# Optimization experiments

Measured on AMD Instinct MI355X. Metric: run time of the kernel, lower is better.

## Reference

```python
import jax, jax.numpy as jnp
from jax import lax
import numpy as np

HID = 1000


def _lstm_cell(x, h, c, W_ih, W_hh, b_ih, b_hh):
    # PyTorch nn.LSTMCell gate order: i, f, g, o
    gates = x @ W_ih.T + b_ih + h @ W_hh.T + b_hh  # [B, 4H]
    i, f, g, o = jnp.split(gates, 4, axis=-1)
    c2 = jax.nn.sigmoid(f) * c + jax.nn.sigmoid(i) * jnp.tanh(g)
    h2 = jax.nn.sigmoid(o) * jnp.tanh(c2)
    return h2, c2


def setup_inputs() -> dict:
    key = jax.random.key(0)
    ks = jax.random.split(key, 8)
    B, T, nbones = 256, 49, 64
    D = nbones * 3
    s = 0.05
    inp = {"enc_in": jax.random.normal(ks[0], (B, T, D), jnp.float32)}
    dims = [D, HID, HID]
    for l in range(3):
        inp[f"W_ih{l}"] = jax.random.normal(ks[1 + 2 * l], (4 * HID, dims[l]), jnp.float32) * s
        inp[f"W_hh{l}"] = jax.random.normal(ks[2 + 2 * l], (4 * HID, HID), jnp.float32) * s
        inp[f"b_ih{l}"] = jnp.zeros((4 * HID,), jnp.float32)
        inp[f"b_hh{l}"] = jnp.zeros((4 * HID,), jnp.float32)
    inp["train"] = 0  # eval mode: dropout is identity
    return inp


def reference(enc_in, W_ih0, W_hh0, b_ih0, b_hh0,
              W_ih1, W_hh1, b_ih1, b_hh1,
              W_ih2, W_hh2, b_ih2, b_hh2, train):
    params = [(W_ih0, W_hh0, b_ih0, b_hh0),
              (W_ih1, W_hh1, b_ih1, b_hh1),
              (W_ih2, W_hh2, b_ih2, b_hh2)]
    B = enc_in.shape[0]
    zeros = jnp.zeros((B, HID), enc_in.dtype)
    init = (tuple(zeros for _ in range(3)), tuple(zeros for _ in range(3)))

    def step(carry, x):
        hs, cs = carry
        new_h, new_c = [], []
        inp = x
        for l in range(3):
            h2, c2 = _lstm_cell(inp, hs[l], cs[l], *params[l])
            new_h.append(h2)
            new_c.append(c2)
            inp = h2  # dropout with train=False is identity
        return (tuple(new_h), tuple(new_c)), jnp.stack(new_h)  # [3, B, H]

    # scan over time: enc_in [B, T, D] -> [T, B, D]
    _, ys = lax.scan(step, init, jnp.transpose(enc_in, (1, 0, 2)))
    # ys: [T, 3, B, H] -> [3, B, T, H]; equals the original per-layer `output`
    out = jnp.transpose(ys, (1, 2, 0, 3))
    return out
```

## Files before the change

kernel.cpp:

```cpp
#include <hip/hip_runtime.h>

#define HID_ 1000
#define NB 256
#define TT 49
#define DIN 192
#define NPAD 1024
#define M_ALL (TT * 256)

typedef _Float16 f16;
typedef _Float16 f16x4 __attribute__((ext_vector_type(4)));
typedef _Float16 f16x8 __attribute__((ext_vector_type(8)));
typedef float f32x4 __attribute__((ext_vector_type(4)));
typedef const __attribute__((address_space(1))) unsigned int* gas_u32;
typedef __attribute__((address_space(3))) unsigned int* las_u32;

__device__ __forceinline__ float sigmf_(float x) {
    return 1.0f / (1.0f + __expf(-x));
}
__device__ __forceinline__ float tanhf_(float x) {
    float ax = fabsf(x);
    float e = __expf(-2.0f * ax);
    float t = (1.0f - e) / (1.0f + e);
    return copysignf(t, x);
}

__global__ void conv_weight(const float* __restrict__ src, f16* __restrict__ dst,
                            int K, int KPADv) {
    size_t total = 4ull * NPAD * KPADv;
    for (size_t idx = (size_t)blockIdx.x * blockDim.x + threadIdx.x; idx < total;
         idx += (size_t)gridDim.x * blockDim.x) {
        int kp = (int)(idx % KPADv);
        size_t rest = idx / KPADv;
        int np = (int)(rest % NPAD);
        int g = (int)(rest / NPAD);
        f16 v = (f16)0.0f;
        if (np < HID_ && kp < K) v = (f16)src[(size_t)(g * HID_ + np) * K + kp];
        dst[idx] = v;
    }
}

__global__ void conv_x(const float* __restrict__ src, f16* __restrict__ dst) {
    size_t total = (size_t)TT * NB * DIN;
    for (size_t idx = (size_t)blockIdx.x * blockDim.x + threadIdx.x; idx < total;
         idx += (size_t)gridDim.x * blockDim.x) {
        int k = (int)(idx % DIN);
        size_t rest = idx / DIN;
        int b = (int)(rest % NB);
        int t = (int)(rest / NB);
        dst[idx] = (f16)src[((size_t)b * TT + t) * DIN + k];
    }
}

__global__ void conv_bias(const float* __restrict__ bih, const float* __restrict__ bhh,
                          float* __restrict__ dst) {
    int idx = blockIdx.x * blockDim.x + threadIdx.x;
    if (idx < 4 * NPAD) {
        int np = idx & (NPAD - 1);
        int g = idx >> 10;
        float v = 0.0f;
        if (np < HID_) v = bih[g * HID_ + np] + bhh[g * HID_ + np];
        dst[idx] = v;
    }
}

__global__ __launch_bounds__(256) void input_gemm(
    const f16* __restrict__ A, int lda, int kiters,
    const f16* __restrict__ W, int ldw,
    const float* __restrict__ bias,
    f16* __restrict__ pre2) {
    __shared__ f16 As[128 * 64];
    __shared__ f16 Bs[128 * 64];
    const int id = blockIdx.x;
    const int sw = (id & 7) * (gridDim.x >> 3) + (id >> 3);
    const int m0 = (sw >> 5) << 7;
    const int n0 = (sw & 31) << 7;
    const int w = threadIdx.x >> 6;
    const int lane = threadIdx.x & 63;
    const int r = lane & 15;
    const int u = lane >> 4;
    const int kb8 = u << 3;
    const int wm = (w >> 1) << 6, wn = (w & 1) << 6;
    const int strow = (w << 5) + (lane >> 3);
    const int stcol = (lane & 7) << 3;

    f32x4 acc[4][4];
#pragma unroll
    for (int i = 0; i < 4; i++)
#pragma unroll
        for (int j = 0; j < 4; j++) acc[i][j] = (f32x4){0.f, 0.f, 0.f, 0.f};

    for (int kt = 0; kt < kiters; kt++) {
        const int k0 = kt << 6;
#pragma unroll
        for (int q = 0; q < 4; q++) {
            const int row = strow + (q << 3);
            const int cbase = ((w << 5) + (q << 3)) << 6;
            const f16* ga = A + (size_t)(m0 + row) * lda + k0 + stcol;
            const f16* gb = W + (size_t)(n0 + row) * ldw + k0 + stcol;
            __builtin_amdgcn_global_load_lds((gas_u32)ga, (las_u32)(As + cbase), 16, 0, 0);
            __builtin_amdgcn_global_load_lds((gas_u32)gb, (las_u32)(Bs + cbase), 16, 0, 0);
        }
        __syncthreads();
#pragma unroll
        for (int ks = 0; ks < 2; ks++) {
            f16x8 av[4], bv[4];
#pragma unroll
            for (int i = 0; i < 4; i++)
                av[i] = *(const f16x8*)(As + ((wm + i * 16 + r) << 6) + (ks << 5) + kb8);
#pragma unroll
            for (int j = 0; j < 4; j++)
                bv[j] = *(const f16x8*)(Bs + ((wn + j * 16 + r) << 6) + (ks << 5) + kb8);
#pragma unroll
            for (int i = 0; i < 4; i++)
#pragma unroll
                for (int j = 0; j < 4; j++)
                    acc[i][j] = __builtin_amdgcn_mfma_f32_16x16x32_f16(av[i], bv[j], acc[i][j], 0, 0, 0);
        }
        __syncthreads();
    }

#pragma unroll
    for (int j = 0; j < 4; j++) {
        const int gcol = n0 + wn + j * 16 + r;
        const float bj = bias[gcol];
        const int g = gcol >> 10;
        const int cl = gcol & 1023;
        const int jt2 = cl >> 5;
        const int n2 = (cl >> 4) & 1;
#pragma unroll
        for (int i = 0; i < 4; i++) {
            const int grow = m0 + wm + i * 16 + (u << 2);
            const int t_ = grow >> 8;
            const int bt2 = (grow >> 5) & 7;
            const int mi = i & 1;
            f16x4 hv;
#pragma unroll
            for (int q = 0; q < 4; q++) hv[q] = (f16)(acc[i][j][q] + bj);
            const int slot = (u << 4) + r;
            *(f16x4*)(pre2 + (((size_t)t_ * 8 + bt2) * 32 + jt2) * 4096 +
                      (size_t)slot * 64 + g * 16 + n2 * 8 + mi * 4) = hv;
        }
    }
}

__global__ __launch_bounds__(512, 2) void rec_persist(
    const f16* __restrict__ Whh, const f16* __restrict__ pre2,
    f16* __restrict__ hall, float* __restrict__ outl,
    unsigned int* __restrict__ flags) {
    __shared__ __align__(16) char smem[64 * 1024];
    __shared__ float pl[4 * 4 * 32 * 34];
    const int bid = blockIdx.x;
    const int bt = bid & 7;
    const int jt = bid >> 3;
    const int b0 = bt << 5;
    const int jc0 = jt << 5;
    const int tid = threadIdx.x;
    const int w = tid >> 6;
    const int gp = w >> 2;
    const int kh = w & 3;
    const int lane = tid & 63;
    const int r = lane & 15;
    const int u = lane >> 4;
    const int swz = (r & 7) << 4;

    f16x8 wreg[2][2][8];
#pragma unroll
    for (int gl = 0; gl < 2; gl++)
#pragma unroll
        for (int n = 0; n < 2; n++) {
            const f16* wp = Whh + ((size_t)((2 * gp + gl) * NPAD + jc0 + n * 16 + r)) * NPAD +
                            (kh << 8) + (u << 3);
#pragma unroll
            for (int ks = 0; ks < 8; ks++) wreg[gl][n][ks] = *(const f16x8*)(wp + ks * 32);
        }

    const int eb = tid >> 4;
    const int ej = (tid & 15) << 1;
    float cv[2] = {0.f, 0.f};
    unsigned int* myflags = flags + bt * TT;
    const size_t preblk = (((size_t)bt * 32 + jt) * 4096) + (size_t)lane * 64 + gp * 32;

    auto LOADP = [&](int tindex, f16x8 (&pc)[4]) {
        if (kh == 0) {
            const f16* pp = pre2 + (size_t)tindex * 8 * 32 * 4096 + preblk;
#pragma unroll
            for (int c = 0; c < 4; c++) pc[c] = *(const f16x8*)(pp + c * 8);
        }
    };

    auto STEP = [&](int t, f16x8 (&pc)[4], f16x8 (&pn)[4]) {
        LOADP(t + 1 < TT ? t + 1 : t, pn);

        if (t > 0) {
            while (__hip_atomic_load(myflags + (t - 1), __ATOMIC_RELAXED,
                                     __HIP_MEMORY_SCOPE_AGENT) < 32u) {}
            asm volatile("" ::: "memory");
            const char* hread = (const char*)(hall + (size_t)(t - 1) * NB * NPAD);
#pragma unroll
            for (int i = 0; i < 8; i++) {
                const int c = tid + (i << 9);
                const int row = c >> 7;
                const int cb = (c & 127) << 4;
                const char* gsrc = hread + ((size_t)(b0 + row) << 11) + (cb ^ ((row & 7) << 4));
                __builtin_amdgcn_global_load_lds((gas_u32)gsrc,
                                                 (las_u32)(smem + (w << 10) + (i << 13)), 16, 0, 0);
            }
        }
        __syncthreads();

        f32x4 acc[2][2][2];
#pragma unroll
        for (int mi = 0; mi < 2; mi++)
#pragma unroll
            for (int gl = 0; gl < 2; gl++)
#pragma unroll
                for (int n = 0; n < 2; n++)
#pragma unroll
                    for (int q = 0; q < 4; q++)
                        acc[mi][gl][n][q] = (kh == 0) ? (float)pc[gl * 2 + n][mi * 4 + q] : 0.f;

        if (t > 0) {
#pragma unroll
            for (int ks = 0; ks < 8; ks++) {
                const int kb = ((kh * 8 + ks) << 6) + (u << 4);
                f16x8 a0 = *(const f16x8*)(smem + r * 2048 + (kb ^ swz));
                f16x8 a1 = *(const f16x8*)(smem + (16 + r) * 2048 + (kb ^ swz));
#pragma unroll
                for (int gl = 0; gl < 2; gl++)
#pragma unroll
                    for (int n = 0; n < 2; n++) {
                        acc[0][gl][n] = __builtin_amdgcn_mfma_f32_16x16x32_f16(
                            a0, wreg[gl][n][ks], acc[0][gl][n], 0, 0, 0);
                        acc[1][gl][n] = __builtin_amdgcn_mfma_f32_16x16x32_f16(
                            a1, wreg[gl][n][ks], acc[1][gl][n], 0, 0, 0);
                    }
            }
        }
#pragma unroll
        for (int mi = 0; mi < 2; mi++)
#pragma unroll
            for (int gl = 0; gl < 2; gl++)
#pragma unroll
                for (int n = 0; n < 2; n++)
#pragma unroll
                    for (int q = 0; q < 4; q++)
                        pl[((kh * 4 + 2 * gp + gl) * 32 + mi * 16 + u * 4 + q) * 34 +
                           n * 16 + r] = acc[mi][gl][n][q];
        __syncthreads();

        float gv[4][2];
#pragma unroll
        for (int gate = 0; gate < 4; gate++) {
            float2 s = make_float2(0.f, 0.f);
#pragma unroll
            for (int k2 = 0; k2 < 4; k2++) {
                float2 p = *(const float2*)&pl[((k2 * 4 + gate) * 32 + eb) * 34 + ej];
                s.x += p.x;
                s.y += p.y;
            }
            gv[gate][0] = s.x;
            gv[gate][1] = s.y;
        }
        float hvv[2];
#pragma unroll
        for (int q = 0; q < 2; q++) {
            float cn = sigmf_(gv[1][q]) * cv[q] + sigmf_(gv[0][q]) * tanhf_(gv[2][q]);
            hvv[q] = sigmf_(gv[3][q]) * tanhf_(cn);
            cv[q] = cn;
        }
        {
            union { f16 h2[2]; unsigned uu; } cvt;
            cvt.h2[0] = (f16)hvv[0];
            cvt.h2[1] = (f16)hvv[1];
            __hip_atomic_store(
                (unsigned*)(hall + ((size_t)t * NB + b0 + eb) * NPAD + jc0 + ej), cvt.uu,
                __ATOMIC_RELAXED, __HIP_MEMORY_SCOPE_AGENT);
        }
        __syncthreads();
        if (tid == 0)
            __hip_atomic_fetch_add(myflags + t, 1u, __ATOMIC_RELAXED, __HIP_MEMORY_SCOPE_AGENT);
        const int col = jc0 + ej;
        if (col < HID_) {
            *(float2*)(outl + ((size_t)(b0 + eb) * TT + t) * HID_ + col) =
                make_float2(hvv[0], hvv[1]);
        }
    };

    f16x8 pA[4] = {}, pB[4] = {};
    LOADP(0, pA);
    for (int t = 0; t < TT; t += 2) {
        STEP(t, pA, pB);
        if (t + 1 < TT) STEP(t + 1, pB, pA);
    }
}

extern "C" void kernel_launch(void* const* d_in, const int* in_sizes, int n_in,
                              void* d_out, int out_size, void* d_ws, size_t ws_size,
                              hipStream_t stream) {
    const float* enc_in = (const float*)d_in[0];
    const float* W_ih[3] = {(const float*)d_in[1], (const float*)d_in[5], (const float*)d_in[9]};
    const float* W_hh[3] = {(const float*)d_in[2], (const float*)d_in[6], (const float*)d_in[10]};
    const float* b_ih[3] = {(const float*)d_in[3], (const float*)d_in[7], (const float*)d_in[11]};
    const float* b_hh[3] = {(const float*)d_in[4], (const float*)d_in[8], (const float*)d_in[12]};
    float* out = (float*)d_out;

    char* ws = (char*)d_ws;
    size_t off = 0;
    auto alloc = [&](size_t bytes) {
        char* p = ws + off;
        off += (bytes + 255) & ~(size_t)255;
        return p;
    };
    f16* Wih_c[3];
    f16* Whh_c[3];
    Wih_c[0] = (f16*)alloc(4ull * NPAD * DIN * sizeof(f16));
    Whh_c[0] = (f16*)alloc(4ull * NPAD * NPAD * sizeof(f16));
    Wih_c[1] = (f16*)alloc(4ull * NPAD * NPAD * sizeof(f16));
    Whh_c[1] = (f16*)alloc(4ull * NPAD * NPAD * sizeof(f16));
    Wih_c[2] = (f16*)alloc(4ull * NPAD * NPAD * sizeof(f16));
    Whh_c[2] = (f16*)alloc(4ull * NPAD * NPAD * sizeof(f16));
    float* bias_c[3];
    for (int l = 0; l < 3; l++) bias_c[l] = (float*)alloc(4ull * NPAD * sizeof(float));
    f16* xbf = (f16*)alloc((size_t)TT * NB * DIN * sizeof(f16));
    f16* hall[3];
    for (int l = 0; l < 3; l++) hall[l] = (f16*)alloc((size_t)TT * NB * NPAD * sizeof(f16));
    f16* pre2 = (f16*)alloc((size_t)M_ALL * 4096 * sizeof(f16));
    unsigned int* flags = (unsigned int*)alloc(3ull * 8 * TT * sizeof(unsigned int));

    hipMemsetAsync(flags, 0, 3ull * 8 * TT * sizeof(unsigned int), stream);

    conv_weight<<<512, 256, 0, stream>>>(W_ih[0], Wih_c[0], DIN, DIN);
    conv_weight<<<2048, 256, 0, stream>>>(W_hh[0], Whh_c[0], HID_, NPAD);
    conv_weight<<<2048, 256, 0, stream>>>(W_ih[1], Wih_c[1], HID_, NPAD);
    conv_weight<<<2048, 256, 0, stream>>>(W_hh[1], Whh_c[1], HID_, NPAD);
    conv_weight<<<2048, 256, 0, stream>>>(W_ih[2], Wih_c[2], HID_, NPAD);
    conv_weight<<<2048, 256, 0, stream>>>(W_hh[2], Whh_c[2], HID_, NPAD);
    conv_x<<<1024, 256, 0, stream>>>(enc_in, xbf);
    for (int l = 0; l < 3; l++)
        conv_bias<<<(4 * NPAD + 255) / 256, 256, 0, stream>>>(b_ih[l], b_hh[l], bias_c[l]);

    for (int l = 0; l < 3; l++) {
        if (l == 0)
            input_gemm<<<3136, 256, 0, stream>>>(xbf, DIN, DIN / 64, Wih_c[0], DIN,
                                                 bias_c[0], pre2);
        else
            input_gemm<<<3136, 256, 0, stream>>>(hall[l - 1], NPAD, NPAD / 64, Wih_c[l], NPAD,
                                                 bias_c[l], pre2);
        rec_persist<<<256, 512, 0, stream>>>(
            Whh_c[l], pre2, hall[l], out + (size_t)l * NB * TT * HID_,
            flags + (size_t)l * 8 * TT);
    }
}
```

Before: 1.268 ms.

## Split recurrent step flags per K-quarter and load h directly into registers

The persistent recurrent kernel now waits on four per-quarter flags, each covering the 8 column-blocks that produce one K-slice, and each flag sits on its own cache line. This replaces a single flag per batch tile that counted all 32 blocks. Each wave waits only for the hidden-state slice it consumes and loads that slice straight from global memory into registers instead of staging the whole h tile in shared memory behind a block-wide barrier. This should shorten the critical path between timesteps. In exchange, h is read without LDS reuse, so each wave issues its own global loads.

```diff
diff --git a/kernel.cpp b/kernel.cpp
--- a/kernel.cpp
+++ b/kernel.cpp
@@ -147,7 +147,6 @@
     const f16* __restrict__ Whh, const f16* __restrict__ pre2,
     f16* __restrict__ hall, float* __restrict__ outl,
     unsigned int* __restrict__ flags) {
-    __shared__ __align__(16) char smem[64 * 1024];
     __shared__ float pl[4 * 4 * 32 * 34];
     const int bid = blockIdx.x;
     const int bt = bid & 7;
@@ -161,7 +160,6 @@
     const int lane = tid & 63;
     const int r = lane & 15;
     const int u = lane >> 4;
-    const int swz = (r & 7) << 4;
 
     f16x8 wreg[2][2][8];
 #pragma unroll
@@ -177,7 +175,7 @@
     const int eb = tid >> 4;
     const int ej = (tid & 15) << 1;
     float cv[2] = {0.f, 0.f};
-    unsigned int* myflags = flags + bt * TT;
+    const size_t fl_base = (size_t)bt * TT * 4 * 32;
     const size_t preblk = (((size_t)bt * 32 + jt) * 4096) + (size_t)lane * 64 + gp * 32;
 
     auto LOADP = [&](int tindex, f16x8 (&pc)[4]) {
@@ -189,25 +187,6 @@
     };
 
     auto STEP = [&](int t, f16x8 (&pc)[4], f16x8 (&pn)[4]) {
-        LOADP(t + 1 < TT ? t + 1 : t, pn);
-
-        if (t > 0) {
-            while (__hip_atomic_load(myflags + (t - 1), __ATOMIC_RELAXED,
-                                     __HIP_MEMORY_SCOPE_AGENT) < 32u) {}
-            asm volatile("" ::: "memory");
-            const char* hread = (const char*)(hall + (size_t)(t - 1) * NB * NPAD);
-#pragma unroll
-            for (int i = 0; i < 8; i++) {
-                const int c = tid + (i << 9);
-                const int row = c >> 7;
-                const int cb = (c & 127) << 4;
-                const char* gsrc = hread + ((size_t)(b0 + row) << 11) + (cb ^ ((row & 7) << 4));
-                __builtin_amdgcn_global_load_lds((gas_u32)gsrc,
-                                                 (las_u32)(smem + (w << 10) + (i << 13)), 16, 0, 0);
-            }
-        }
-        __syncthreads();
-
         f32x4 acc[2][2][2];
 #pragma unroll
         for (int mi = 0; mi < 2; mi++)
@@ -219,23 +198,34 @@
                     for (int q = 0; q < 4; q++)
                         acc[mi][gl][n][q] = (kh == 0) ? (float)pc[gl * 2 + n][mi * 4 + q] : 0.f;
 
+        LOADP(t + 1 < TT ? t + 1 : t, pn);
+
         if (t > 0) {
+            const unsigned* fq = flags + fl_base + ((size_t)(t - 1) * 4 + kh) * 32;
+            while (__hip_atomic_load(fq, __ATOMIC_RELAXED, __HIP_MEMORY_SCOPE_AGENT) < 8u) {}
+            asm volatile("" ::: "memory");
+            const f16* hr = hall + (size_t)(t - 1) * NB * NPAD + (size_t)b0 * NPAD +
+                            (kh << 8) + (u << 3);
+            f16x8 hreg[2][8];
 #pragma unroll
             for (int ks = 0; ks < 8; ks++) {
-                const int kb = ((kh * 8 + ks) << 6) + (u << 4);
-                f16x8 a0 = *(const f16x8*)(smem + r * 2048 + (kb ^ swz));
-                f16x8 a1 = *(const f16x8*)(smem + (16 + r) * 2048 + (kb ^ swz));
+                hreg[0][ks] = *(const f16x8*)(hr + (size_t)r * NPAD + ks * 32);
+                hreg[1][ks] = *(const f16x8*)(hr + (size_t)(16 + r) * NPAD + ks * 32);
+            }
+#pragma unroll
+            for (int ks = 0; ks < 8; ks++) {
 #pragma unroll
                 for (int gl = 0; gl < 2; gl++)
 #pragma unroll
                     for (int n = 0; n < 2; n++) {
                         acc[0][gl][n] = __builtin_amdgcn_mfma_f32_16x16x32_f16(
-                            a0, wreg[gl][n][ks], acc[0][gl][n], 0, 0, 0);
+                            hreg[0][ks], wreg[gl][n][ks], acc[0][gl][n], 0, 0, 0);
                         acc[1][gl][n] = __builtin_amdgcn_mfma_f32_16x16x32_f16(
-                            a1, wreg[gl][n][ks], acc[1][gl][n], 0, 0, 0);
+                            hreg[1][ks], wreg[gl][n][ks], acc[1][gl][n], 0, 0, 0);
                     }
             }
         }
+
 #pragma unroll
         for (int mi = 0; mi < 2; mi++)
 #pragma unroll
@@ -278,7 +268,8 @@
         }
         __syncthreads();
         if (tid == 0)
-            __hip_atomic_fetch_add(myflags + t, 1u, __ATOMIC_RELAXED, __HIP_MEMORY_SCOPE_AGENT);
+            __hip_atomic_fetch_add(flags + fl_base + ((size_t)t * 4 + (jt >> 3)) * 32, 1u,
+                                   __ATOMIC_RELAXED, __HIP_MEMORY_SCOPE_AGENT);
         const int col = jc0 + ej;
         if (col < HID_) {
             *(float2*)(outl + ((size_t)(b0 + eb) * TT + t) * HID_ + col) =
@@ -325,9 +316,10 @@
     f16* hall[3];
     for (int l = 0; l < 3; l++) hall[l] = (f16*)alloc((size_t)TT * NB * NPAD * sizeof(f16));
     f16* pre2 = (f16*)alloc((size_t)M_ALL * 4096 * sizeof(f16));
-    unsigned int* flags = (unsigned int*)alloc(3ull * 8 * TT * sizeof(unsigned int));
-
-    hipMemsetAsync(flags, 0, 3ull * 8 * TT * sizeof(unsigned int), stream);
+    const size_t fl_layer = (size_t)8 * TT * 4 * 32;
+    unsigned int* flags = (unsigned int*)alloc(3 * fl_layer * sizeof(unsigned int));
+
+    hipMemsetAsync(flags, 0, 3 * fl_layer * sizeof(unsigned int), stream);
 
     conv_weight<<<512, 256, 0, stream>>>(W_ih[0], Wih_c[0], DIN, DIN);
     conv_weight<<<2048, 256, 0, stream>>>(W_hh[0], Whh_c[0], HID_, NPAD);
@@ -348,6 +340,6 @@
                                                  bias_c[l], pre2);
         rec_persist<<<256, 512, 0, stream>>>(
             Whh_c[l], pre2, hall[l], out + (size_t)l * NB * TT * HID_,
-            flags + (size_t)l * 8 * TT);
-    }
-}
+            flags + (size_t)l * fl_layer);
+    }
+}
```

New measurement: 1.439 ms. +13.5%, slower.
